# Kernel optimization log

Hardware: AMD Instinct MI355X
Metric: run time of the kernel (lower is better)

Reference implementation:

```python
import jax, jax.numpy as jnp
import numpy as np

B, S, D, H = 4, 1024, 1024, 16
DK = D // H
EPS_LN = 1e-6

def setup_inputs() -> dict:
    key = jax.random.key(0)
    ks = jax.random.split(key, 16)
    sc = 1.0 / np.sqrt(D)
    inp = {}
    names = ['q_r','q_i','k_r','k_i','v_r','v_i']
    for i, n in enumerate(names):
        inp[n] = jax.random.normal(ks[i], (B, S, D), dtype=jnp.float32)
    wnames = ['wq_r','wq_i','wk_r','wk_i','wv_r','wv_i','wfc_r','wfc_i']
    for i, n in enumerate(wnames):
        inp[n] = jax.random.normal(ks[6 + i], (D, D), dtype=jnp.float32) * sc
    inp['gamma'] = jnp.ones((D,), dtype=jnp.float32)
    inp['beta'] = jnp.zeros((D,), dtype=jnp.float32)
    return inp

def _clinear(xr, xi, wr, wi):
    # complex (xr + i*xi) @ (wr + i*wi)^T, weights stored [out, in]
    r = xr @ wr.T - xi @ wi.T
    im = xi @ wr.T + xr @ wi.T
    return r, im

def _forward(q_r, q_i, k_r, k_i, v_r, v_i, wq_r, wq_i, wk_r, wk_i,
             wv_r, wv_i, wfc_r, wfc_i, gamma, beta):
    res_r, res_i = q_r, q_i
    qr, qi = _clinear(q_r, q_i, wq_r, wq_i)
    kr, ki = _clinear(k_r, k_i, wk_r, wk_i)
    vr, vi = _clinear(v_r, v_i, wv_r, wv_i)
    # [B,S,D] -> [B,H,S,DK]
    split = lambda x: x.reshape(B, S, H, DK).transpose(0, 2, 1, 3)
    qr, qi, kr, ki, vr, vi = map(split, (qr, qi, kr, ki, vr, vi))
    temp = jnp.asarray(DK ** 0.5, qr.dtype)
    qr = qr / temp
    qi = qi / temp
    # q @ conj(k)^T : real = qr.kr + qi.ki ; imag = qi.kr - qr.ki
    ar = jnp.einsum('bhqd,bhkd->bhqk', qr, kr) + jnp.einsum('bhqd,bhkd->bhqk', qi, ki)
    ai = jnp.einsum('bhqd,bhkd->bhqk', qi, kr) - jnp.einsum('bhqd,bhkd->bhqk', qr, ki)
    attn = jax.nn.softmax(jnp.sqrt(ar * ar + ai * ai), axis=-1)  # magnitude softmax
    or_ = jnp.einsum('bhqk,bhkd->bhqd', attn, vr)
    oi_ = jnp.einsum('bhqk,bhkd->bhqd', attn, vi)
    merge = lambda x: x.transpose(0, 2, 1, 3).reshape(B, S, D)
    or_, oi_ = merge(or_), merge(oi_)
    fr, fi = _clinear(or_, oi_, wfc_r, wfc_i)
    # ComplexDropout in eval mode: identity except imag += 1e-10
    fi = fi + 1e-10
    xr = fr + res_r
    xi = fi + res_i
    # ComplexLayerNorm: mean over all non-batch dims, elementwise magnitude norm
    mr = jnp.mean(xr, axis=(1, 2), keepdims=True)
    mi = jnp.mean(xi, axis=(1, 2), keepdims=True)
    cr = xr - mr
    ci = xi - mi
    std = jnp.sqrt(cr * cr + ci * ci + EPS_LN)
    yr = gamma * (cr / std) + beta
    yi = gamma * (ci / std)
    return yr, yi, attn

def reference(q_r, q_i, k_r, k_i, v_r, v_i, wq_r, wq_i, wk_r, wk_i,
              wv_r, wv_i, wfc_r, wfc_i, gamma, beta):
    return _forward(q_r, q_i, k_r, k_i, v_r, v_i, wq_r, wq_i, wk_r, wk_i,
                    wv_r, wv_i, wfc_r, wfc_i, gamma, beta)
```

## Files before the change

kernel.cpp:

```cpp
#include <hip/hip_runtime.h>
#include <math.h>

#define NB 4
#define SEQ 1024
#define DIM 1024
#define NH 16
#define DHEAD 64
#define BUFN 4194304ULL
#define WHN  1048576ULL
#define LOG2E 1.4426950408889634f

typedef _Float16 f16x8 __attribute__((ext_vector_type(8)));
typedef _Float16 f16x4 __attribute__((ext_vector_type(4)));
typedef float    f32x4 __attribute__((ext_vector_type(4)));

#define MFMA16 __builtin_amdgcn_mfma_f32_16x16x32_f16

__device__ __forceinline__ void split4(const float4 v, f16x4& h, f16x4& l)
{
    const _Float16 h0=(_Float16)v.x, h1=(_Float16)v.y, h2=(_Float16)v.z, h3=(_Float16)v.w;
    h = (f16x4){h0, h1, h2, h3};
    l = (f16x4){(_Float16)((v.x-(float)h0)*2048.0f),
                (_Float16)((v.y-(float)h1)*2048.0f),
                (_Float16)((v.z-(float)h2)*2048.0f),
                (_Float16)((v.w-(float)h3)*2048.0f)};
}

__global__ __launch_bounds__(256)
void splitx_kernel(const float* __restrict__ xr, const float* __restrict__ xi,
                   _Float16* __restrict__ XS)
{
    const float* x = blockIdx.y ? xi : xr;
    _Float16* h = XS + (size_t)blockIdx.y * 2 * BUFN;
    _Float16* l = h + BUFN;
    const int i = (blockIdx.x * 256 + threadIdx.x) << 2;
    const float4 v = *(const float4*)(x + i);
    f16x4 hh, ll; split4(v, hh, ll);
    *(f16x4*)(h + i) = hh;
    *(f16x4*)(l + i) = ll;
}

__global__ __launch_bounds__(256)
void splitw_kernel(const float* w0, const float* w1, const float* w2, const float* w3,
                   const float* w4, const float* w5, const float* w6, const float* w7,
                   _Float16* __restrict__ WS)
{
    const int y = blockIdx.y;
    const float* x = (y==0)?w0:(y==1)?w1:(y==2)?w2:(y==3)?w3:(y==4)?w4:(y==5)?w5:(y==6)?w6:w7;
    _Float16* h = WS + (size_t)y * 2 * WHN;
    _Float16* l = h + WHN;
    const int i = (blockIdx.x * 256 + threadIdx.x) << 2;
    float4 v = *(const float4*)(x + i);
    v.x *= 64.0f; v.y *= 64.0f; v.z *= 64.0f; v.w *= 64.0f;
    f16x4 hh, ll; split4(v, hh, ll);
    *(f16x4*)(h + i) = hh;
    *(f16x4*)(l + i) = ll;
}

template<int MODE>
__global__ __launch_bounds__(256, 1)
void cgemm16_kernel(const _Float16* __restrict__ Ahr, const _Float16* __restrict__ Alr,
                    const _Float16* __restrict__ Ahi, const _Float16* __restrict__ Ali,
                    const _Float16* __restrict__ Bhr, const _Float16* __restrict__ Blr,
                    const _Float16* __restrict__ Bhi, const _Float16* __restrict__ Bli,
                    float* __restrict__ outr, float* __restrict__ outi,
                    const float* __restrict__ resr, const float* __restrict__ resi,
                    float* __restrict__ msum, float scale)
{
    __shared__ __align__(16) _Float16 As[4][64][40];
    __shared__ __align__(16) _Float16 Bs[4][64][40];
    const int t    = threadIdx.x;
    const int lane = t & 63;
    const int w    = t >> 6;
    const int wm   = w >> 1, wn = w & 1;
    const int lr   = lane & 15;
    const int kc   = (lane >> 4) << 3;
    const int m0   = blockIdx.x * 64;
    const int o0   = blockIdx.y * 64;
    const int srow = t >> 2;
    const int sc8  = (t & 3) << 3;

    const size_t aoff = (size_t)(m0 + srow) * DIM + sc8;
    const size_t boff = (size_t)(o0 + srow) * DIM + sc8;

    f32x4 acc[2][2][4];
    #pragma unroll
    for (int i = 0; i < 2; ++i)
        #pragma unroll
        for (int j = 0; j < 2; ++j)
            #pragma unroll
            for (int c = 0; c < 4; ++c)
                acc[i][j][c] = (f32x4){0.f, 0.f, 0.f, 0.f};

    for (int k0 = 0; k0 < DIM; k0 += 32) {
        const uint4 va0 = *(const uint4*)(Ahr + aoff + k0);
        const uint4 va1 = *(const uint4*)(Alr + aoff + k0);
        const uint4 va2 = *(const uint4*)(Ahi + aoff + k0);
        const uint4 va3 = *(const uint4*)(Ali + aoff + k0);
        const uint4 vb0 = *(const uint4*)(Bhr + boff + k0);
        const uint4 vb1 = *(const uint4*)(Blr + boff + k0);
        const uint4 vb2 = *(const uint4*)(Bhi + boff + k0);
        const uint4 vb3 = *(const uint4*)(Bli + boff + k0);
        __syncthreads();
        *(uint4*)&As[0][srow][sc8] = va0;
        *(uint4*)&As[1][srow][sc8] = va1;
        *(uint4*)&As[2][srow][sc8] = va2;
        *(uint4*)&As[3][srow][sc8] = va3;
        *(uint4*)&Bs[0][srow][sc8] = vb0;
        *(uint4*)&Bs[1][srow][sc8] = vb1;
        *(uint4*)&Bs[2][srow][sc8] = vb2;
        *(uint4*)&Bs[3][srow][sc8] = vb3;
        __syncthreads();

        f16x8 a0[2], a1[2], a2[2], a3[2];
        #pragma unroll
        for (int mt = 0; mt < 2; ++mt) {
            const int ar = wm * 32 + mt * 16 + lr;
            a0[mt] = *(const f16x8*)&As[0][ar][kc];
            a1[mt] = *(const f16x8*)&As[1][ar][kc];
            a2[mt] = *(const f16x8*)&As[2][ar][kc];
            a3[mt] = *(const f16x8*)&As[3][ar][kc];
        }
        #pragma unroll
        for (int nt = 0; nt < 2; ++nt) {
            const int br = wn * 32 + nt * 16 + lr;
            const f16x8 bhr = *(const f16x8*)&Bs[0][br][kc];
            const f16x8 blr = *(const f16x8*)&Bs[1][br][kc];
            const f16x8 bhi = *(const f16x8*)&Bs[2][br][kc];
            const f16x8 bli = *(const f16x8*)&Bs[3][br][kc];
            const f16x8 bhiN = -bhi;
            const f16x8 bliN = -bli;
            #pragma unroll
            for (int mt = 0; mt < 2; ++mt) {
                acc[mt][nt][0] = MFMA16(a0[mt], bhr,  acc[mt][nt][0], 0, 0, 0);
                acc[mt][nt][0] = MFMA16(a2[mt], bhiN, acc[mt][nt][0], 0, 0, 0);
                acc[mt][nt][1] = MFMA16(a0[mt], blr,  acc[mt][nt][1], 0, 0, 0);
                acc[mt][nt][1] = MFMA16(a1[mt], bhr,  acc[mt][nt][1], 0, 0, 0);
                acc[mt][nt][1] = MFMA16(a2[mt], bliN, acc[mt][nt][1], 0, 0, 0);
                acc[mt][nt][1] = MFMA16(a3[mt], bhiN, acc[mt][nt][1], 0, 0, 0);
                acc[mt][nt][2] = MFMA16(a2[mt], bhr,  acc[mt][nt][2], 0, 0, 0);
                acc[mt][nt][2] = MFMA16(a0[mt], bhi,  acc[mt][nt][2], 0, 0, 0);
                acc[mt][nt][3] = MFMA16(a2[mt], blr,  acc[mt][nt][3], 0, 0, 0);
                acc[mt][nt][3] = MFMA16(a3[mt], bhr,  acc[mt][nt][3], 0, 0, 0);
                acc[mt][nt][3] = MFMA16(a0[mt], bli,  acc[mt][nt][3], 0, 0, 0);
                acc[mt][nt][3] = MFMA16(a1[mt], bhi,  acc[mt][nt][3], 0, 0, 0);
            }
        }
    }

    const float INVL = 1.0f / 2048.0f;
    if (MODE == 0) {
        #pragma unroll
        for (int mt = 0; mt < 2; ++mt)
            #pragma unroll
            for (int nt = 0; nt < 2; ++nt)
                #pragma unroll
                for (int r = 0; r < 4; ++r) {
                    const int mrow = m0 + wm * 32 + mt * 16 + ((lane >> 4)) * 4 + r;
                    const int ncol = o0 + wn * 32 + nt * 16 + lr;
                    const float cr = (acc[mt][nt][0][r] + acc[mt][nt][1][r] * INVL) * scale;
                    const float ci = (acc[mt][nt][2][r] + acc[mt][nt][3][r] * INVL) * scale;
                    const int b = mrow >> 10, s = mrow & 1023, h = ncol >> 6, dk = ncol & 63;
                    const size_t idx = (((size_t)b * NH + h) * SEQ + s) * DHEAD + dk;
                    outr[idx] = cr;
                    outi[idx] = ci;
                }
    } else {
        float sr = 0.f, si = 0.f;
        #pragma unroll
        for (int mt = 0; mt < 2; ++mt)
            #pragma unroll
            for (int nt = 0; nt < 2; ++nt)
                #pragma unroll
                for (int r = 0; r < 4; ++r) {
                    const int mrow = m0 + wm * 32 + mt * 16 + ((lane >> 4)) * 4 + r;
                    const int ncol = o0 + wn * 32 + nt * 16 + lr;
                    const size_t idx = (size_t)mrow * DIM + ncol;
                    const float cr = (acc[mt][nt][0][r] + acc[mt][nt][1][r] * INVL) * scale
                                     + resr[idx];
                    const float ci = (acc[mt][nt][2][r] + acc[mt][nt][3][r] * INVL) * scale
                                     + 1e-10f + resi[idx];
                    outr[idx] = cr;
                    outi[idx] = ci;
                    sr += cr; si += ci;
                }
        #pragma unroll
        for (int off = 32; off > 0; off >>= 1) { sr += __shfl_xor(sr, off); si += __shfl_xor(si, off); }
        __shared__ float wsum[8];
        if ((t & 63) == 0) { wsum[w * 2 + 0] = sr; wsum[w * 2 + 1] = si; }
        __syncthreads();
        if (t == 0) {
            atomicAdd(&msum[2 * (m0 >> 10) + 0], wsum[0] + wsum[2] + wsum[4] + wsum[6]);
            atomicAdd(&msum[2 * (m0 >> 10) + 1], wsum[1] + wsum[3] + wsum[5] + wsum[7]);
        }
    }
}

__global__ __launch_bounds__(256)
void vtrans_kernel(const float* __restrict__ VR, const float* __restrict__ VI,
                   _Float16* __restrict__ Trh, _Float16* __restrict__ Trl,
                   _Float16* __restrict__ Tih, _Float16* __restrict__ Til)
{
    __shared__ float sr[64][68];
    __shared__ float si[64][68];
    const int t = threadIdx.x;
    const int kb = blockIdx.x, bh = blockIdx.y;
    const size_t ibase = (size_t)bh * SEQ * DHEAD + (size_t)kb * 64 * DHEAD;
    const int row = t >> 4, c0 = (t & 15) << 2;
    #pragma unroll
    for (int it = 0; it < 4; ++it) {
        const float4 a = *(const float4*)(VR + ibase + (size_t)(row + 16*it) * DHEAD + c0);
        const float4 b = *(const float4*)(VI + ibase + (size_t)(row + 16*it) * DHEAD + c0);
        *(float4*)&sr[row + 16*it][c0] = a;
        *(float4*)&si[row + 16*it][c0] = b;
    }
    __syncthreads();
    const int dk = t >> 2, k0 = (t & 3) << 4;
    f16x8 hr[2], lr8[2], hi8[2], li8[2];
    #pragma unroll
    for (int kk = 0; kk < 16; ++kk) {
        const float xr = sr[k0 + kk][dk];
        const float xi = si[k0 + kk][dk];
        const _Float16 hxr = (_Float16)xr;
        const _Float16 hxi = (_Float16)xi;
        hr[kk>>3][kk&7]  = hxr;
        lr8[kk>>3][kk&7] = (_Float16)((xr - (float)hxr) * 2048.0f);
        hi8[kk>>3][kk&7] = hxi;
        li8[kk>>3][kk&7] = (_Float16)((xi - (float)hxi) * 2048.0f);
    }
    const size_t ob = ((size_t)bh * 64 + dk) * SEQ + kb * 64 + k0;
    *(f16x8*)(Trh + ob) = hr[0];  *(f16x8*)(Trh + ob + 8) = hr[1];
    *(f16x8*)(Trl + ob) = lr8[0]; *(f16x8*)(Trl + ob + 8) = lr8[1];
    *(f16x8*)(Tih + ob) = hi8[0]; *(f16x8*)(Tih + ob + 8) = hi8[1];
    *(f16x8*)(Til + ob) = li8[0]; *(f16x8*)(Til + ob + 8) = li8[1];
}

__global__ __launch_bounds__(256, 1)
void attn_scores_kernel(const float* __restrict__ QR, const float* __restrict__ QI,
                        const float* __restrict__ KR, const float* __restrict__ KI,
                        float* __restrict__ attn, float* __restrict__ Lbuf)
{
    __shared__ __align__(16) _Float16 Ks[4][64][72];
    __shared__ float red[2][64];
    const int t = threadIdx.x;
    const int lane = t & 63;
    const int w = t >> 6, wm = w >> 1, wn = w & 1;
    const int lr = lane & 15, g = lane >> 4, kc = g << 3;
    const int q0 = blockIdx.x * 64;
    const int bh = blockIdx.y;
    const size_t base = (size_t)bh * SEQ * DHEAD;
    const int srow = t >> 2, sc0 = (t & 3) << 4;

    #pragma unroll
    for (int c = 0; c < 4; ++c) {
        const float4 a = *(const float4*)(QR + base + (size_t)(q0 + srow) * DHEAD + sc0 + 4*c);
        const float4 b = *(const float4*)(QI + base + (size_t)(q0 + srow) * DHEAD + sc0 + 4*c);
        f16x4 h, l;
        split4(a, h, l);
        *(f16x4*)&Ks[0][srow][sc0 + 4*c] = h;
        *(f16x4*)&Ks[1][srow][sc0 + 4*c] = l;
        split4(b, h, l);
        *(f16x4*)&Ks[2][srow][sc0 + 4*c] = h;
        *(f16x4*)&Ks[3][srow][sc0 + 4*c] = l;
    }
    __syncthreads();
    f16x8 qhr[2][2], qlr[2][2], qhi[2][2], qli[2][2];
    #pragma unroll
    for (int mt = 0; mt < 2; ++mt) {
        const int row = wm * 32 + mt * 16 + lr;
        #pragma unroll
        for (int ks = 0; ks < 2; ++ks) {
            const int col = ks * 32 + kc;
            qhr[mt][ks] = *(const f16x8*)&Ks[0][row][col];
            qlr[mt][ks] = *(const f16x8*)&Ks[1][row][col];
            qhi[mt][ks] = *(const f16x8*)&Ks[2][row][col];
            qli[mt][ks] = *(const f16x8*)&Ks[3][row][col];
        }
    }

    float lsum[2][4] = {};
    float4 pr[4], pi4[4];
    #pragma unroll
    for (int c = 0; c < 4; ++c) {
        pr[c]  = *(const float4*)(KR + base + (size_t)srow * DHEAD + sc0 + 4*c);
        pi4[c] = *(const float4*)(KI + base + (size_t)srow * DHEAD + sc0 + 4*c);
    }

    for (int kt = 0; kt < 16; ++kt) {
        __syncthreads();
        #pragma unroll
        for (int c = 0; c < 4; ++c) {
            f16x4 h, l;
            split4(pr[c], h, l);
            *(f16x4*)&Ks[0][srow][sc0 + 4*c] = h;
            *(f16x4*)&Ks[1][srow][sc0 + 4*c] = l;
            split4(pi4[c], h, l);
            *(f16x4*)&Ks[2][srow][sc0 + 4*c] = h;
            *(f16x4*)&Ks[3][srow][sc0 + 4*c] = l;
        }
        __syncthreads();
        if (kt < 15) {
            const size_t koff = base + (size_t)((kt + 1) * 64 + srow) * DHEAD;
            #pragma unroll
            for (int c = 0; c < 4; ++c) {
                pr[c]  = *(const float4*)(KR + koff + sc0 + 4*c);
                pi4[c] = *(const float4*)(KI + koff + sc0 + 4*c);
            }
        }
        f32x4 arh[2][2], arl[2][2], aih[2][2], ail[2][2];
        #pragma unroll
        for (int i = 0; i < 2; ++i)
            #pragma unroll
            for (int j = 0; j < 2; ++j) {
                arh[i][j] = (f32x4){0,0,0,0}; arl[i][j] = (f32x4){0,0,0,0};
                aih[i][j] = (f32x4){0,0,0,0}; ail[i][j] = (f32x4){0,0,0,0};
            }
        #pragma unroll
        for (int nt = 0; nt < 2; ++nt) {
            const int brow = wn * 32 + nt * 16 + lr;
            #pragma unroll
            for (int ks = 0; ks < 2; ++ks) {
                const int col = ks * 32 + kc;
                const f16x8 khr = *(const f16x8*)&Ks[0][brow][col];
                const f16x8 klr = *(const f16x8*)&Ks[1][brow][col];
                const f16x8 khi = *(const f16x8*)&Ks[2][brow][col];
                const f16x8 kli = *(const f16x8*)&Ks[3][brow][col];
                const f16x8 khiN = -khi;
                const f16x8 kliN = -kli;
                #pragma unroll
                for (int mt = 0; mt < 2; ++mt) {
                    arh[mt][nt] = MFMA16(qhr[mt][ks], khr,  arh[mt][nt], 0,0,0);
                    arh[mt][nt] = MFMA16(qhi[mt][ks], khi,  arh[mt][nt], 0,0,0);
                    arl[mt][nt] = MFMA16(qhr[mt][ks], klr,  arl[mt][nt], 0,0,0);
                    arl[mt][nt] = MFMA16(qlr[mt][ks], khr,  arl[mt][nt], 0,0,0);
                    arl[mt][nt] = MFMA16(qhi[mt][ks], kli,  arl[mt][nt], 0,0,0);
                    arl[mt][nt] = MFMA16(qli[mt][ks], khi,  arl[mt][nt], 0,0,0);
                    aih[mt][nt] = MFMA16(qhi[mt][ks], khr,  aih[mt][nt], 0,0,0);
                    aih[mt][nt] = MFMA16(qhr[mt][ks], khiN, aih[mt][nt], 0,0,0);
                    ail[mt][nt] = MFMA16(qhi[mt][ks], klr,  ail[mt][nt], 0,0,0);
                    ail[mt][nt] = MFMA16(qli[mt][ks], khr,  ail[mt][nt], 0,0,0);
                    ail[mt][nt] = MFMA16(qhr[mt][ks], kliN, ail[mt][nt], 0,0,0);
                    ail[mt][nt] = MFMA16(qlr[mt][ks], khiN, ail[mt][nt], 0,0,0);
                }
            }
        }
        const float INV = 1.0f / 2048.0f;
        #pragma unroll
        for (int mt = 0; mt < 2; ++mt)
            #pragma unroll
            for (int nt = 0; nt < 2; ++nt)
                #pragma unroll
                for (int r = 0; r < 4; ++r) {
                    const float ar = arh[mt][nt][r] + arl[mt][nt][r] * INV;
                    const float ai = aih[mt][nt][r] + ail[mt][nt][r] * INV;
                    const float m2 = ar * ar + ai * ai;
                    const float s  = m2 * __frsqrt_rn(m2 + 1e-30f);
                    const float pp = exp2f(s * LOG2E);
                    const int q = q0 + wm * 32 + mt * 16 + g * 4 + r;
                    const int k = kt * 64 + wn * 32 + nt * 16 + lr;
                    attn[((size_t)bh * SEQ + q) * SEQ + k] = pp;
                    lsum[mt][r] += pp;
                }
    }
    #pragma unroll
    for (int mt = 0; mt < 2; ++mt)
        #pragma unroll
        for (int r = 0; r < 4; ++r) {
            float v = lsum[mt][r];
            v += __shfl_xor(v, 1); v += __shfl_xor(v, 2);
            v += __shfl_xor(v, 4); v += __shfl_xor(v, 8);
            lsum[mt][r] = v;
        }
    if (lr == 0) {
        #pragma unroll
        for (int mt = 0; mt < 2; ++mt)
            #pragma unroll
            for (int r = 0; r < 4; ++r)
                red[wn][wm * 32 + mt * 16 + g * 4 + r] = lsum[mt][r];
    }
    __syncthreads();
    if (t < 64) Lbuf[(size_t)bh * SEQ + q0 + t] = red[0][t] + red[1][t];
}

__global__ __launch_bounds__(256, 1)
void attn_pv_kernel(float* __restrict__ attn, const float* __restrict__ Lbuf,
                    const _Float16* __restrict__ Trh, const _Float16* __restrict__ Trl,
                    const _Float16* __restrict__ Tih, const _Float16* __restrict__ Til,
                    _Float16* __restrict__ XOhr, _Float16* __restrict__ XOlr,
                    _Float16* __restrict__ XOhi, _Float16* __restrict__ XOli)
{
    __shared__ __align__(16) _Float16 Psh[2][64][72];
    __shared__ __align__(16) _Float16 Psl[2][64][72];
    __shared__ float invL[64];
    const int t = threadIdx.x;
    const int lane = t & 63;
    const int w = t >> 6, wm = w >> 1, wn = w & 1;
    const int lr = lane & 15, g = lane >> 4, kc = g << 3;
    const int q0 = blockIdx.x * 64;
    const int bh = blockIdx.y;
    const size_t abase = ((size_t)bh * SEQ + q0) * SEQ;
    const size_t vbase = (size_t)bh * 64 * SEQ;

    if (t < 64) invL[t] = 1.0f / Lbuf[(size_t)bh * SEQ + q0 + t];

    const size_t voff[2] = { vbase + (size_t)(wn * 32 + lr) * SEQ + kc,
                             vbase + (size_t)(wn * 32 + 16 + lr) * SEQ + kc };

    f32x4 orh[2][2], orl[2][2], oih[2][2], oil[2][2];
    #pragma unroll
    for (int i = 0; i < 2; ++i)
        #pragma unroll
        for (int j = 0; j < 2; ++j) {
            orh[i][j] = (f32x4){0,0,0,0}; orl[i][j] = (f32x4){0,0,0,0};
            oih[i][j] = (f32x4){0,0,0,0}; oil[i][j] = (f32x4){0,0,0,0};
        }

    const int prow = t >> 4, pcol = (t & 15) << 2;
    float4 sc[2][4];
    #pragma unroll
    for (int u = 0; u < 2; ++u)
        #pragma unroll
        for (int it = 0; it < 4; ++it)
            sc[u][it] = *(const float4*)(attn + abase + (size_t)(prow + 16*it) * SEQ
                                         + u * 64 + pcol);

    for (int kp = 0; kp < 8; ++kp) {
        __syncthreads();
        #pragma unroll
        for (int u = 0; u < 2; ++u)
            #pragma unroll
            for (int it = 0; it < 4; ++it) {
                const int row = prow + 16*it;
                const float inv = invL[row];
                float4 p;
                p.x = sc[u][it].x * inv;
                p.y = sc[u][it].y * inv;
                p.z = sc[u][it].z * inv;
                p.w = sc[u][it].w * inv;
                *(float4*)(attn + abase + (size_t)row * SEQ + (kp*2 + u) * 64 + pcol) = p;
                float4 ps;
                ps.x = p.x * 1024.0f; ps.y = p.y * 1024.0f;
                ps.z = p.z * 1024.0f; ps.w = p.w * 1024.0f;
                f16x4 h, l; split4(ps, h, l);
                *(f16x4*)&Psh[u][row][pcol] = h;
                *(f16x4*)&Psl[u][row][pcol] = l;
            }
        __syncthreads();
        if (kp < 7) {
            #pragma unroll
            for (int u = 0; u < 2; ++u)
                #pragma unroll
                for (int it = 0; it < 4; ++it)
                    sc[u][it] = *(const float4*)(attn + abase + (size_t)(prow + 16*it) * SEQ
                                                 + (kp*2 + 2 + u) * 64 + pcol);
        }
        #pragma unroll
        for (int u = 0; u < 2; ++u) {
            #pragma unroll
            for (int ks = 0; ks < 2; ++ks) {
                const int col = ks * 32 + kc;
                f16x8 ph[2], pl[2];
                #pragma unroll
                for (int mt = 0; mt < 2; ++mt) {
                    const int row = wm * 32 + mt * 16 + lr;
                    ph[mt] = *(const f16x8*)&Psh[u][row][col];
                    pl[mt] = *(const f16x8*)&Psl[u][row][col];
                }
                const size_t vcol = (size_t)((kp*2 + u) * 64 + ks * 32);
                #pragma unroll
                for (int nt = 0; nt < 2; ++nt) {
                    const size_t vo = voff[nt] + vcol;
                    const f16x8 vhr = *(const f16x8*)(Trh + vo);
                    const f16x8 vlr = *(const f16x8*)(Trl + vo);
                    const f16x8 vhi = *(const f16x8*)(Tih + vo);
                    const f16x8 vli = *(const f16x8*)(Til + vo);
                    #pragma unroll
                    for (int mt = 0; mt < 2; ++mt) {
                        orh[mt][nt] = MFMA16(ph[mt], vhr, orh[mt][nt], 0,0,0);
                        orl[mt][nt] = MFMA16(ph[mt], vlr, orl[mt][nt], 0,0,0);
                        orl[mt][nt] = MFMA16(pl[mt], vhr, orl[mt][nt], 0,0,0);
                        oih[mt][nt] = MFMA16(ph[mt], vhi, oih[mt][nt], 0,0,0);
                        oil[mt][nt] = MFMA16(ph[mt], vli, oil[mt][nt], 0,0,0);
                        oil[mt][nt] = MFMA16(pl[mt], vhi, oil[mt][nt], 0,0,0);
                    }
                }
            }
        }
    }
    const float IL = 1.0f / 2048.0f, SP = 1.0f / 1024.0f;
    const int b = bh >> 4, h = bh & 15;
    #pragma unroll
    for (int mt = 0; mt < 2; ++mt)
        #pragma unroll
        for (int nt = 0; nt < 2; ++nt)
            #pragma unroll
            for (int r = 0; r < 4; ++r) {
                const float orv = (orh[mt][nt][r] + orl[mt][nt][r] * IL) * SP;
                const float oiv = (oih[mt][nt][r] + oil[mt][nt][r] * IL) * SP;
                const int q  = q0 + wm * 32 + mt * 16 + g * 4 + r;
                const int dk = wn * 32 + nt * 16 + lr;
                const size_t addr = ((size_t)b * SEQ + q) * DIM + h * DHEAD + dk;
                _Float16 hh = (_Float16)orv;
                XOhr[addr] = hh;
                XOlr[addr] = (_Float16)((orv - (float)hh) * 2048.0f);
                hh = (_Float16)oiv;
                XOhi[addr] = hh;
                XOli[addr] = (_Float16)((oiv - (float)hh) * 2048.0f);
            }
}

__global__ __launch_bounds__(256)
void ln_kernel(const float* __restrict__ xr, const float* __restrict__ xi,
               const float* __restrict__ msum, const float* __restrict__ gamma,
               const float* __restrict__ beta,
               float* __restrict__ yr, float* __restrict__ yi)
{
    const int gid = blockIdx.x * 256 + threadIdx.x;
    const int flat = gid << 2;
    const int b = flat >> 20;
    const int d = flat & (DIM - 1);
    const float mr = msum[2*b+0] * (1.0f/1048576.0f);
    const float mi = msum[2*b+1] * (1.0f/1048576.0f);
    const float4 vr = *(const float4*)(xr + flat);
    const float4 vi = *(const float4*)(xi + flat);
    const float4 g  = *(const float4*)(gamma + d);
    const float4 bt = *(const float4*)(beta + d);
    float4 or4, oi4;
    {
        float cr = vr.x - mr, ci = vi.x - mi;
        float inv = 1.0f / sqrtf(cr*cr + ci*ci + 1e-6f);
        or4.x = g.x * (cr * inv) + bt.x; oi4.x = g.x * (ci * inv);
    }
    {
        float cr = vr.y - mr, ci = vi.y - mi;
        float inv = 1.0f / sqrtf(cr*cr + ci*ci + 1e-6f);
        or4.y = g.y * (cr * inv) + bt.y; oi4.y = g.y * (ci * inv);
    }
    {
        float cr = vr.z - mr, ci = vi.z - mi;
        float inv = 1.0f / sqrtf(cr*cr + ci*ci + 1e-6f);
        or4.z = g.z * (cr * inv) + bt.z; oi4.z = g.z * (ci * inv);
    }
    {
        float cr = vr.w - mr, ci = vi.w - mi;
        float inv = 1.0f / sqrtf(cr*cr + ci*ci + 1e-6f);
        or4.w = g.w * (cr * inv) + bt.w; oi4.w = g.w * (ci * inv);
    }
    *(float4*)(yr + flat) = or4;
    *(float4*)(yi + flat) = oi4;
}

extern "C" void kernel_launch(void* const* d_in, const int* in_sizes, int n_in,
                              void* d_out, int out_size, void* d_ws, size_t ws_size,
                              hipStream_t stream)
{
    const float* q_r   = (const float*)d_in[0];
    const float* q_i   = (const float*)d_in[1];
    const float* k_r   = (const float*)d_in[2];
    const float* k_i   = (const float*)d_in[3];
    const float* v_r   = (const float*)d_in[4];
    const float* v_i   = (const float*)d_in[5];
    const float* wq_r  = (const float*)d_in[6];
    const float* wq_i  = (const float*)d_in[7];
    const float* wk_r  = (const float*)d_in[8];
    const float* wk_i  = (const float*)d_in[9];
    const float* wv_r  = (const float*)d_in[10];
    const float* wv_i  = (const float*)d_in[11];
    const float* wfc_r = (const float*)d_in[12];
    const float* wfc_i = (const float*)d_in[13];
    const float* gamma = (const float*)d_in[14];
    const float* beta  = (const float*)d_in[15];

    float* ws = (float*)d_ws;
    const size_t BUF = BUFN;
    float* QR   = ws + 0*BUF;
    float* QI   = ws + 1*BUF;
    float* KR   = ws + 2*BUF;
    float* KI   = ws + 3*BUF;
    float* VR   = ws + 4*BUF;
    float* VI   = ws + 5*BUF;
    float* MSUM = ws + 6*BUF;
    float* LBUF = ws + 6*BUF + 16;
    _Float16* F  = (_Float16*)(ws + 6*BUF + 16 + 65536);
    _Float16* XS = F;
    _Float16* VT = F + 4*BUF;
    _Float16* WSp = F + 8*BUF;
    float* XR = QR;
    float* XI = QI;

    float* yr   = (float*)d_out;
    float* yi   = yr + BUF;
    float* attn = yr + 2*BUF;

    const dim3 blk(256);
    const dim3 g_gemm(64, 16);
    const float IWS = 1.0f / 64.0f;

    splitw_kernel<<<dim3(1024, 8), blk, 0, stream>>>(wq_r, wq_i, wk_r, wk_i,
                                                     wv_r, wv_i, wfc_r, wfc_i, WSp);

    splitx_kernel<<<dim3(4096, 2), blk, 0, stream>>>(q_r, q_i, XS);
    cgemm16_kernel<0><<<g_gemm, blk, 0, stream>>>(
        XS + 0*BUF, XS + 1*BUF, XS + 2*BUF, XS + 3*BUF,
        WSp + 0*WHN, WSp + 1*WHN, WSp + 2*WHN, WSp + 3*WHN,
        QR, QI, nullptr, nullptr, nullptr, 0.125f * IWS);

    splitx_kernel<<<dim3(4096, 2), blk, 0, stream>>>(k_r, k_i, XS);
    cgemm16_kernel<0><<<g_gemm, blk, 0, stream>>>(
        XS + 0*BUF, XS + 1*BUF, XS + 2*BUF, XS + 3*BUF,
        WSp + 4*WHN, WSp + 5*WHN, WSp + 6*WHN, WSp + 7*WHN,
        KR, KI, nullptr, nullptr, nullptr, IWS);

    splitx_kernel<<<dim3(4096, 2), blk, 0, stream>>>(v_r, v_i, XS);
    cgemm16_kernel<0><<<g_gemm, blk, 0, stream>>>(
        XS + 0*BUF, XS + 1*BUF, XS + 2*BUF, XS + 3*BUF,
        WSp + 8*WHN, WSp + 9*WHN, WSp + 10*WHN, WSp + 11*WHN,
        VR, VI, nullptr, nullptr, nullptr, IWS);

    vtrans_kernel<<<dim3(16, 64), blk, 0, stream>>>(VR, VI,
        VT + 0*BUF, VT + 1*BUF, VT + 2*BUF, VT + 3*BUF);

    attn_scores_kernel<<<dim3(16, 64), blk, 0, stream>>>(QR, QI, KR, KI, attn, LBUF);

    attn_pv_kernel<<<dim3(16, 64), blk, 0, stream>>>(attn, LBUF,
        VT + 0*BUF, VT + 1*BUF, VT + 2*BUF, VT + 3*BUF,
        XS + 0*BUF, XS + 1*BUF, XS + 2*BUF, XS + 3*BUF);

    hipMemsetAsync(MSUM, 0, 8 * sizeof(float), stream);
    cgemm16_kernel<1><<<g_gemm, blk, 0, stream>>>(
        XS + 0*BUF, XS + 1*BUF, XS + 2*BUF, XS + 3*BUF,
        WSp + 12*WHN, WSp + 13*WHN, WSp + 14*WHN, WSp + 15*WHN,
        XR, XI, q_r, q_i, MSUM, IWS);
    ln_kernel<<<dim3(4096), blk, 0, stream>>>(XR, XI, MSUM, gamma, beta, yr, yi);
}
```

Measured before the change: 995.5 us.

## Software-pipeline PV kernel: normalize next P tile while MFMAs consume current

Restructures the attention-PV loop into a ping-pong pipeline over the two shared P buffers. The normalize, store and split of the next 64-column tile overlaps with the MFMAs on the current tile, and global loads of scores are issued one tile ahead. The aim is to hide the global write/read and conversion latency behind matrix work, so MFMAs no longer sit idle between the two barriers. It keeps the same number of barriers per tile but adds register pressure from the extra prefetched score set.

```diff
diff --git a/kernel.cpp b/kernel.cpp
--- a/kernel.cpp
+++ b/kernel.cpp
@@ -382,6 +382,60 @@
     if (t < 64) Lbuf[(size_t)bh * SEQ + q0 + t] = red[0][t] + red[1][t];
 }
 
+#define PV_LOAD(KT, SCSET)                                                     \
+    _Pragma("unroll")                                                          \
+    for (int it = 0; it < 4; ++it)                                             \
+        SCSET[it] = *(const float4*)(attn + abase                              \
+                     + (size_t)(prow + 16*it) * SEQ + (KT) * 64 + pcol);
+
+#define PV_NORM(KT, SCSET, BUF)                                                \
+    _Pragma("unroll")                                                          \
+    for (int it = 0; it < 4; ++it) {                                           \
+        const int row_ = prow + 16*it;                                         \
+        const float inv_ = invL[row_];                                         \
+        float4 p_;                                                             \
+        p_.x = SCSET[it].x * inv_; p_.y = SCSET[it].y * inv_;                  \
+        p_.z = SCSET[it].z * inv_; p_.w = SCSET[it].w * inv_;                  \
+        *(float4*)(attn + abase + (size_t)row_ * SEQ + (KT) * 64 + pcol) = p_; \
+        float4 ps_;                                                            \
+        ps_.x = p_.x * 1024.0f; ps_.y = p_.y * 1024.0f;                        \
+        ps_.z = p_.z * 1024.0f; ps_.w = p_.w * 1024.0f;                        \
+        f16x4 h_, l_; split4(ps_, h_, l_);                                     \
+        *(f16x4*)&Psh[BUF][row_][pcol] = h_;                                   \
+        *(f16x4*)&Psl[BUF][row_][pcol] = l_;                                   \
+    }
+
+#define PV_MFMA(BUF, KT)                                                       \
+    _Pragma("unroll")                                                          \
+    for (int ks = 0; ks < 2; ++ks) {                                           \
+        const int col_ = ks * 32 + kc;                                         \
+        f16x8 ph_[2], pl_[2];                                                  \
+        _Pragma("unroll")                                                      \
+        for (int mt = 0; mt < 2; ++mt) {                                       \
+            const int row_ = wm * 32 + mt * 16 + lr;                           \
+            ph_[mt] = *(const f16x8*)&Psh[BUF][row_][col_];                    \
+            pl_[mt] = *(const f16x8*)&Psl[BUF][row_][col_];                    \
+        }                                                                      \
+        const size_t vcol_ = (size_t)((KT) * 64 + ks * 32);                    \
+        _Pragma("unroll")                                                      \
+        for (int nt = 0; nt < 2; ++nt) {                                       \
+            const size_t vo_ = voff[nt] + vcol_;                               \
+            const f16x8 vhr_ = *(const f16x8*)(Trh + vo_);                     \
+            const f16x8 vlr_ = *(const f16x8*)(Trl + vo_);                     \
+            const f16x8 vhi_ = *(const f16x8*)(Tih + vo_);                     \
+            const f16x8 vli_ = *(const f16x8*)(Til + vo_);                     \
+            _Pragma("unroll")                                                  \
+            for (int mt = 0; mt < 2; ++mt) {                                   \
+                orh[mt][nt] = MFMA16(ph_[mt], vhr_, orh[mt][nt], 0,0,0);       \
+                orl[mt][nt] = MFMA16(ph_[mt], vlr_, orl[mt][nt], 0,0,0);       \
+                orl[mt][nt] = MFMA16(pl_[mt], vhr_, orl[mt][nt], 0,0,0);       \
+                oih[mt][nt] = MFMA16(ph_[mt], vhi_, oih[mt][nt], 0,0,0);       \
+                oil[mt][nt] = MFMA16(ph_[mt], vli_, oil[mt][nt], 0,0,0);       \
+                oil[mt][nt] = MFMA16(pl_[mt], vhi_, oil[mt][nt], 0,0,0);       \
+            }                                                                  \
+        }                                                                      \
+    }
+
 __global__ __launch_bounds__(256, 1)
 void attn_pv_kernel(float* __restrict__ attn, const float* __restrict__ Lbuf,
                     const _Float16* __restrict__ Trh, const _Float16* __restrict__ Trl,
@@ -416,77 +470,28 @@
         }
 
     const int prow = t >> 4, pcol = (t & 15) << 2;
-    float4 sc[2][4];
-    #pragma unroll
-    for (int u = 0; u < 2; ++u)
-        #pragma unroll
-        for (int it = 0; it < 4; ++it)
-            sc[u][it] = *(const float4*)(attn + abase + (size_t)(prow + 16*it) * SEQ
-                                         + u * 64 + pcol);
+    float4 scA[4], scB[4];
+
+    PV_LOAD(0, scA);
+    __syncthreads();
+    PV_NORM(0, scA, 0);
+    PV_LOAD(1, scB);
+    __syncthreads();
 
     for (int kp = 0; kp < 8; ++kp) {
-        __syncthreads();
-        #pragma unroll
-        for (int u = 0; u < 2; ++u)
-            #pragma unroll
-            for (int it = 0; it < 4; ++it) {
-                const int row = prow + 16*it;
-                const float inv = invL[row];
-                float4 p;
-                p.x = sc[u][it].x * inv;
-                p.y = sc[u][it].y * inv;
-                p.z = sc[u][it].z * inv;
-                p.w = sc[u][it].w * inv;
-                *(float4*)(attn + abase + (size_t)row * SEQ + (kp*2 + u) * 64 + pcol) = p;
-                float4 ps;
-                ps.x = p.x * 1024.0f; ps.y = p.y * 1024.0f;
-                ps.z = p.z * 1024.0f; ps.w = p.w * 1024.0f;
-                f16x4 h, l; split4(ps, h, l);
-                *(f16x4*)&Psh[u][row][pcol] = h;
-                *(f16x4*)&Psl[u][row][pcol] = l;
-            }
+        const int ktA = kp * 2;
+        PV_NORM(ktA + 1, scB, 1);
+        if (kp < 7) { PV_LOAD(ktA + 2, scA); }
+        PV_MFMA(0, ktA);
         __syncthreads();
         if (kp < 7) {
-            #pragma unroll
-            for (int u = 0; u < 2; ++u)
-                #pragma unroll
-                for (int it = 0; it < 4; ++it)
-                    sc[u][it] = *(const float4*)(attn + abase + (size_t)(prow + 16*it) * SEQ
-                                                 + (kp*2 + 2 + u) * 64 + pcol);
-        }
-        #pragma unroll
-        for (int u = 0; u < 2; ++u) {
-            #pragma unroll
-            for (int ks = 0; ks < 2; ++ks) {
-                const int col = ks * 32 + kc;
-                f16x8 ph[2], pl[2];
-                #pragma unroll
-                for (int mt = 0; mt < 2; ++mt) {
-                    const int row = wm * 32 + mt * 16 + lr;
-                    ph[mt] = *(const f16x8*)&Psh[u][row][col];
-                    pl[mt] = *(const f16x8*)&Psl[u][row][col];
-                }
-                const size_t vcol = (size_t)((kp*2 + u) * 64 + ks * 32);
-                #pragma unroll
-                for (int nt = 0; nt < 2; ++nt) {
-                    const size_t vo = voff[nt] + vcol;
-                    const f16x8 vhr = *(const f16x8*)(Trh + vo);
-                    const f16x8 vlr = *(const f16x8*)(Trl + vo);
-                    const f16x8 vhi = *(const f16x8*)(Tih + vo);
-                    const f16x8 vli = *(const f16x8*)(Til + vo);
-                    #pragma unroll
-                    for (int mt = 0; mt < 2; ++mt) {
-                        orh[mt][nt] = MFMA16(ph[mt], vhr, orh[mt][nt], 0,0,0);
-                        orl[mt][nt] = MFMA16(ph[mt], vlr, orl[mt][nt], 0,0,0);
-                        orl[mt][nt] = MFMA16(pl[mt], vhr, orl[mt][nt], 0,0,0);
-                        oih[mt][nt] = MFMA16(ph[mt], vhi, oih[mt][nt], 0,0,0);
-                        oil[mt][nt] = MFMA16(ph[mt], vli, oil[mt][nt], 0,0,0);
-                        oil[mt][nt] = MFMA16(pl[mt], vhi, oil[mt][nt], 0,0,0);
-                    }
-                }
-            }
-        }
-    }
+            PV_NORM(ktA + 2, scA, 0);
+            PV_LOAD(ktA + 3, scB);
+        }
+        PV_MFMA(1, ktA + 1);
+        __syncthreads();
+    }
+
     const float IL = 1.0f / 2048.0f, SP = 1.0f / 1024.0f;
     const int b = bh >> 4, h = bh & 15;
     #pragma unroll
```

Measured after the change: 995.1 us. About the same (-0.0%).
